# Optimization experiments

Hardware: AMD Instinct MI355X
Metric: run time of the kernel (lower is better)

The kernel has to match this reference:

```python
import jax, jax.numpy as jnp
import numpy as np

B, K, D = 512, 36, 1024
N_KERNELS = 4
OUT_DIM = 1024
OUT_PER_KERNEL = OUT_DIM // N_KERNELS  # 256


def setup_inputs() -> dict:
    key = jax.random.key(0)
    k1, k2, k3, k4, k5 = jax.random.split(key, 5)
    neighbourhood_features = jax.random.normal(k1, (B, K, D), dtype=jnp.float32)
    region_relation_weights = jax.random.uniform(k2, (B, K, K), dtype=jnp.float32)
    # Gaussian mixture params: init uniform(0, 1) as in init_parameters()
    mean_relation = jax.random.uniform(k3, (N_KERNELS,), dtype=jnp.float32)
    precision_relation = jax.random.uniform(k4, (N_KERNELS,), dtype=jnp.float32)
    # Per-kernel Linear weights (bias=False), torch default init U(-1/sqrt(D), 1/sqrt(D))
    bound = 1.0 / np.sqrt(D)
    W = jax.random.uniform(k5, (N_KERNELS, OUT_PER_KERNEL, D), dtype=jnp.float32,
                           minval=-bound, maxval=bound)
    return {
        "neighbourhood_features": neighbourhood_features,
        "region_relation_weights": region_relation_weights,
        "mean_relation": mean_relation,
        "precision_relation": precision_relation,
        "W": W,
    }


def reference(neighbourhood_features, region_relation_weights, mean_relation,
              precision_relation, W):
    b, k, d = neighbourhood_features.shape
    # Gaussian mixture edge weights, normalized over kernels: [B,K,K,n_kernels]
    diff = (region_relation_weights[..., None] - mean_relation) ** 2
    w = jnp.exp(-0.5 * diff / (1e-14 + precision_relation ** 2))
    w = w / jnp.sum(w, axis=-1, keepdims=True)
    # Original repeats feat[b,i] over the neighbour axis j, so
    # bmm(w^T, repeated_feat)[b,i,k,:] == (sum_j w[b,i,j,k]) * feat[b,i,:].
    # Exploit that linearity instead of materializing the [B,K,K,D] repeat.
    ws = jnp.sum(w, axis=2)  # [B,K,n_kernels]
    weighted = ws[..., None] * neighbourhood_features[:, :, None, :]  # [B,K,n,D]
    # Per-kernel linear (stacked): [B,K,n_kernels,out_per_kernel]
    out = jnp.einsum('bknd,nod->bkno', weighted, W)
    # Concatenate kernel outputs -> [B,K,out_feat_dim]
    return out.reshape(b, k, -1)
```

## Files before the change

kernel.cpp:

```cpp
#include <hip/hip_runtime.h>
#include <stdint.h>

#define BB   512
#define KNB  36
#define DD   1024
#define MM   (BB*KNB)
#define NN   1024

typedef float  f32x4  __attribute__((ext_vector_type(4)));
typedef __bf16 bf16x8 __attribute__((ext_vector_type(8)));
typedef unsigned short u16;
typedef unsigned int   u32;

__device__ __forceinline__ u16 f2bf(float f) {
    u32 u = __float_as_uint(f);
    u32 r = (u + 0x7fffu + ((u >> 16) & 1u)) >> 16;
    return (u16)r;
}

__device__ __forceinline__ void gld16(const void* g, void* l) {
    __builtin_amdgcn_global_load_lds(
        (const __attribute__((address_space(1))) u32*)g,
        (__attribute__((address_space(3))) u32*)l,
        16, 0, 0);
}

__device__ __forceinline__ void cast_chunk_swz(const float* __restrict__ in,
                                               u16* __restrict__ out,
                                               long long c, int r) {
    long long src = (c & ~7LL) | ((c & 7) ^ (r & 7));
    const f32x4* p = (const f32x4*)(in + src * 8);
    f32x4 v0 = p[0], v1 = p[1];
    union { u16 us[8]; uint4 u4; } pk;
    pk.us[0] = f2bf(v0.x); pk.us[1] = f2bf(v0.y);
    pk.us[2] = f2bf(v0.z); pk.us[3] = f2bf(v0.w);
    pk.us[4] = f2bf(v1.x); pk.us[5] = f2bf(v1.y);
    pk.us[6] = f2bf(v1.z); pk.us[7] = f2bf(v1.w);
    *((uint4*)(out + c * 8)) = pk.u4;
}

#define WS_BLOCKS   72
#define CW_BLOCKS   512
#define CA_BLOCKS   1152
#define CA_THREADS  (CA_BLOCKS * 256)
__global__ void prep_kernel(const float* __restrict__ rrw,
                            const float* __restrict__ mean,
                            const float* __restrict__ prec,
                            float* __restrict__ wsT,
                            const float* __restrict__ W,
                            u16* __restrict__ Wbf,
                            const float* __restrict__ A,
                            u16* __restrict__ Abf) {
    const int blk = blockIdx.x;
    if (blk < WS_BLOCKS) {
        int id = blk * 256 + threadIdx.x;
        float m0 = mean[0], m1 = mean[1], m2 = mean[2], m3 = mean[3];
        float i0 = 1.0f / (1e-14f + prec[0] * prec[0]);
        float i1 = 1.0f / (1e-14f + prec[1] * prec[1]);
        float i2 = 1.0f / (1e-14f + prec[2] * prec[2]);
        float i3 = 1.0f / (1e-14f + prec[3] * prec[3]);
        const float* p = rrw + (size_t)id * KNB;
        float a0 = 0.f, a1 = 0.f, a2 = 0.f, a3 = 0.f;
        for (int j = 0; j < KNB; ++j) {
            float x = p[j];
            float d0 = x - m0, d1 = x - m1, d2 = x - m2, d3 = x - m3;
            float e0 = expf(-0.5f * d0 * d0 * i0);
            float e1 = expf(-0.5f * d1 * d1 * i1);
            float e2 = expf(-0.5f * d2 * d2 * i2);
            float e3 = expf(-0.5f * d3 * d3 * i3);
            float inv = 1.0f / (e0 + e1 + e2 + e3);
            a0 += e0 * inv; a1 += e1 * inv; a2 += e2 * inv; a3 += e3 * inv;
        }
        wsT[0 * MM + id] = a0;
        wsT[1 * MM + id] = a1;
        wsT[2 * MM + id] = a2;
        wsT[3 * MM + id] = a3;
    } else if (blk < WS_BLOCKS + CW_BLOCKS) {
        long long c = (long long)(blk - WS_BLOCKS) * 256 + threadIdx.x;
        int r = (int)(c >> 7);
        cast_chunk_swz(W, Wbf, c, r);
    } else {
        long long t = (long long)(blk - WS_BLOCKS - CW_BLOCKS) * 256 + threadIdx.x;
#pragma unroll
        for (int k = 0; k < 8; ++k) {
            long long c = t + (long long)k * CA_THREADS;
            int r = (int)(c >> 7);
            cast_chunk_swz(A, Abf, c, r);
        }
    }
}

#define BM 128
#define BN 128
#define BK 64
#define KTILES (DD / BK)

#define VMCNT8()  asm volatile("s_waitcnt vmcnt(8)" ::: "memory")
#define VMCNT0()  asm volatile("s_waitcnt vmcnt(0)" ::: "memory")
#define BAR()     __builtin_amdgcn_s_barrier()

__global__ __launch_bounds__(256, 4) void gemm_kernel(
        const u16* __restrict__ A,
        const u16* __restrict__ Bm,
        const float* __restrict__ wsT,
        float* __restrict__ out) {
    __shared__ __align__(16) u16 As0[BM * BK];
    __shared__ __align__(16) u16 As1[BM * BK];
    __shared__ __align__(16) u16 Bs0[BN * BK];
    __shared__ __align__(16) u16 Bs1[BN * BK];

    const int tid = threadIdx.x;
    const int bid   = blockIdx.x;
    const int xcd   = bid & 7;
    const int local = bid >> 3;
    const int by    = xcd * 18 + (local >> 3);
    const int bx    = local & 7;
    const int rowBase = by * BM;
    const int colBase = bx * BN;
    const int lane = tid & 63;
    const int w    = tid >> 6;
    const int wr   = w >> 1;
    const int wc   = w & 1;
    const int fr   = lane & 15;
    const int fq   = lane >> 4;

    f32x4 acc[4][4];
#pragma unroll
    for (int m = 0; m < 4; ++m)
#pragma unroll
        for (int n = 0; n < 4; ++n)
            acc[m][n] = (f32x4)0.0f;

    const u16* aptr = A  + (size_t)(rowBase + (tid >> 3)) * DD + (tid & 7) * 8;
    const u16* bptr = Bm + (size_t)(colBase + (tid >> 3)) * DD + (tid & 7) * 8;

    auto STAGE = [&](u16* as, u16* bs, int kt) {
#pragma unroll
        for (int i = 0; i < 4; ++i) {
            gld16(aptr + (size_t)i * 32 * DD + kt * BK, &as[(i * 256 + tid) * 8]);
            gld16(bptr + (size_t)i * 32 * DD + kt * BK, &bs[(i * 256 + tid) * 8]);
        }
    };

    auto COMPUTE = [&](const u16* as, const u16* bs) {
#pragma unroll
        for (int kk = 0; kk < 2; ++kk) {
            bf16x8 af[4], bfv[4];
#pragma unroll
            for (int m = 0; m < 4; ++m) {
                int r = wr * 64 + m * 16 + fr;
                int g = kk * 4 + fq;
                af[m] = ((const bf16x8*)&as[r * BK])[g ^ (r & 7)];
            }
#pragma unroll
            for (int n = 0; n < 4; ++n) {
                int r = wc * 64 + n * 16 + fr;
                int g = kk * 4 + fq;
                bfv[n] = ((const bf16x8*)&bs[r * BK])[g ^ (r & 7)];
            }
#pragma unroll
            for (int m = 0; m < 4; ++m)
#pragma unroll
                for (int n = 0; n < 4; ++n)
                    acc[m][n] = __builtin_amdgcn_mfma_f32_16x16x32_bf16(
                        af[m], bfv[n], acc[m][n], 0, 0, 0);
        }
    };

    STAGE(As0, Bs0, 0);

    for (int k2 = 0; k2 < (KTILES - 2) / 2; ++k2) {
        STAGE(As1, Bs1, 2 * k2 + 1);
        VMCNT8();
        BAR();
        COMPUTE(As0, Bs0);
        BAR();
        STAGE(As0, Bs0, 2 * k2 + 2);
        VMCNT8();
        BAR();
        COMPUTE(As1, Bs1);
        BAR();
    }
    STAGE(As1, Bs1, KTILES - 1);
    VMCNT8();
    BAR();
    COMPUTE(As0, Bs0);
    VMCNT0();
    BAR();
    COMPUTE(As1, Bs1);

    const int kn = bx >> 1;
#pragma unroll
    for (int m = 0; m < 4; ++m) {
        int r0 = rowBase + wr * 64 + m * 16 + fq * 4;
        f32x4 s = *(const f32x4*)&wsT[(size_t)kn * MM + r0];
#pragma unroll
        for (int n = 0; n < 4; ++n) {
            int c = colBase + wc * 64 + n * 16 + fr;
            float* o = out + (size_t)r0 * NN + c;
            o[0 * NN] = acc[m][n][0] * s[0];
            o[1 * NN] = acc[m][n][1] * s[1];
            o[2 * NN] = acc[m][n][2] * s[2];
            o[3 * NN] = acc[m][n][3] * s[3];
        }
    }
}

extern "C" void kernel_launch(void* const* d_in, const int* in_sizes, int n_in,
                              void* d_out, int out_size, void* d_ws, size_t ws_size,
                              hipStream_t stream) {
    const float* feat = (const float*)d_in[0];
    const float* rrw  = (const float*)d_in[1];
    const float* mean = (const float*)d_in[2];
    const float* prec = (const float*)d_in[3];
    const float* W    = (const float*)d_in[4];
    float* out = (float*)d_out;

    char* ws = (char*)d_ws;
    float* wsT = (float*)ws;
    u16*   Wbf = (u16*)(ws + 294912);
    u16*   Abf = (u16*)(ws + 294912 + 2097152);

    prep_kernel<<<dim3(WS_BLOCKS + CW_BLOCKS + CA_BLOCKS), dim3(256), 0, stream>>>(
        rrw, mean, prec, wsT, W, Wbf, feat, Abf);
    gemm_kernel<<<dim3((MM / BM) * (NN / BN)), dim3(256), 0, stream>>>(Abf, Wbf, wsT, out);
}
```

Baseline: 72.80 us.

## Fuse fp32-to-bf16 activation cast into GEMM A-tile loads

Removes the separate prep pass that cast the 512x36x1024 fp32 features to bf16 in workspace. The GEMM now loads fp32 A rows into registers, converts them to bf16 and writes them into swizzled LDS after each compute step, while B still streams through global_load_lds. This drops a full write plus re-read of the bf16 activation copy. In exchange, A staging goes through registers, adding VGPR pressure (launch bounds lowered to 2 waves per SIMD) and extra waitcnt and barrier ordering in the pipeline.

```diff
diff --git a/kernel.cpp b/kernel.cpp
--- a/kernel.cpp
+++ b/kernel.cpp
@@ -23,6 +23,13 @@
         (const __attribute__((address_space(1))) u32*)g,
         (__attribute__((address_space(3))) u32*)l,
         16, 0, 0);
+}
+
+__device__ __forceinline__ bf16x8 cvt8(f32x4 lo, f32x4 hi) {
+    bf16x8 r;
+    r[0] = (__bf16)lo.x; r[1] = (__bf16)lo.y; r[2] = (__bf16)lo.z; r[3] = (__bf16)lo.w;
+    r[4] = (__bf16)hi.x; r[5] = (__bf16)hi.y; r[6] = (__bf16)hi.z; r[7] = (__bf16)hi.w;
+    return r;
 }
 
 __device__ __forceinline__ void cast_chunk_swz(const float* __restrict__ in,
@@ -41,16 +48,12 @@
 
 #define WS_BLOCKS   72
 #define CW_BLOCKS   512
-#define CA_BLOCKS   1152
-#define CA_THREADS  (CA_BLOCKS * 256)
 __global__ void prep_kernel(const float* __restrict__ rrw,
                             const float* __restrict__ mean,
                             const float* __restrict__ prec,
                             float* __restrict__ wsT,
                             const float* __restrict__ W,
-                            u16* __restrict__ Wbf,
-                            const float* __restrict__ A,
-                            u16* __restrict__ Abf) {
+                            u16* __restrict__ Wbf) {
     const int blk = blockIdx.x;
     if (blk < WS_BLOCKS) {
         int id = blk * 256 + threadIdx.x;
@@ -75,18 +78,10 @@
         wsT[1 * MM + id] = a1;
         wsT[2 * MM + id] = a2;
         wsT[3 * MM + id] = a3;
-    } else if (blk < WS_BLOCKS + CW_BLOCKS) {
+    } else {
         long long c = (long long)(blk - WS_BLOCKS) * 256 + threadIdx.x;
         int r = (int)(c >> 7);
         cast_chunk_swz(W, Wbf, c, r);
-    } else {
-        long long t = (long long)(blk - WS_BLOCKS - CW_BLOCKS) * 256 + threadIdx.x;
-#pragma unroll
-        for (int k = 0; k < 8; ++k) {
-            long long c = t + (long long)k * CA_THREADS;
-            int r = (int)(c >> 7);
-            cast_chunk_swz(A, Abf, c, r);
-        }
     }
 }
 
@@ -95,12 +90,13 @@
 #define BK 64
 #define KTILES (DD / BK)
 
-#define VMCNT8()  asm volatile("s_waitcnt vmcnt(8)" ::: "memory")
+#define VMCNT12() asm volatile("s_waitcnt vmcnt(12)" ::: "memory")
 #define VMCNT0()  asm volatile("s_waitcnt vmcnt(0)" ::: "memory")
+#define LGKM0()   asm volatile("s_waitcnt lgkmcnt(0)" ::: "memory")
 #define BAR()     __builtin_amdgcn_s_barrier()
 
-__global__ __launch_bounds__(256, 4) void gemm_kernel(
-        const u16* __restrict__ A,
+__global__ __launch_bounds__(256, 2) void gemm_kernel(
+        const float* __restrict__ A,
         const u16* __restrict__ Bm,
         const float* __restrict__ wsT,
         float* __restrict__ out) {
@@ -131,14 +127,31 @@
         for (int n = 0; n < 4; ++n)
             acc[m][n] = (f32x4)0.0f;
 
-    const u16* aptr = A  + (size_t)(rowBase + (tid >> 3)) * DD + (tid & 7) * 8;
-    const u16* bptr = Bm + (size_t)(colBase + (tid >> 3)) * DD + (tid & 7) * 8;
-
-    auto STAGE = [&](u16* as, u16* bs, int kt) {
+    const int ar0 = tid >> 3;
+    const int aj  = tid & 7;
+    const float* abase = A + (size_t)(rowBase + ar0) * DD + aj * 8;
+    const u16*   bptr  = Bm + (size_t)(colBase + ar0) * DD + aj * 8;
+
+    f32x4 ra[4][2];
+
+    auto ISSUE_B = [&](u16* bs, int kt) {
+#pragma unroll
+        for (int i = 0; i < 4; ++i)
+            gld16(bptr + (size_t)i * 32 * DD + kt * BK, &bs[(i * 256 + tid) * 8]);
+    };
+    auto ISSUE_A = [&](int kt) {
 #pragma unroll
         for (int i = 0; i < 4; ++i) {
-            gld16(aptr + (size_t)i * 32 * DD + kt * BK, &as[(i * 256 + tid) * 8]);
-            gld16(bptr + (size_t)i * 32 * DD + kt * BK, &bs[(i * 256 + tid) * 8]);
+            const float* src = abase + (size_t)i * 32 * DD + kt * BK;
+            ra[i][0] = *(const f32x4*)src;
+            ra[i][1] = *(const f32x4*)(src + 4);
+        }
+    };
+    auto WRITE_A = [&](u16* as) {
+#pragma unroll
+        for (int i = 0; i < 4; ++i) {
+            int r = i * 32 + ar0;
+            *(bf16x8*)&as[r * BK + (aj ^ (r & 7)) * 8] = cvt8(ra[i][0], ra[i][1]);
         }
     };
 
@@ -167,24 +180,37 @@
         }
     };
 
-    STAGE(As0, Bs0, 0);
+    ISSUE_B(Bs0, 0);
+    ISSUE_A(0);
+    WRITE_A(As0);
+    VMCNT0(); LGKM0();
+    BAR();
 
     for (int k2 = 0; k2 < (KTILES - 2) / 2; ++k2) {
-        STAGE(As1, Bs1, 2 * k2 + 1);
-        VMCNT8();
+        ISSUE_B(Bs1, 2 * k2 + 1);
+        ISSUE_A(2 * k2 + 1);
+        VMCNT12();
         BAR();
         COMPUTE(As0, Bs0);
-        BAR();
-        STAGE(As0, Bs0, 2 * k2 + 2);
-        VMCNT8();
+        WRITE_A(As1);
+        LGKM0();
+        BAR();
+        ISSUE_B(Bs0, 2 * k2 + 2);
+        ISSUE_A(2 * k2 + 2);
+        VMCNT12();
         BAR();
         COMPUTE(As1, Bs1);
+        WRITE_A(As0);
+        LGKM0();
         BAR();
     }
-    STAGE(As1, Bs1, KTILES - 1);
-    VMCNT8();
+    ISSUE_B(Bs1, KTILES - 1);
+    ISSUE_A(KTILES - 1);
+    VMCNT12();
     BAR();
     COMPUTE(As0, Bs0);
+    WRITE_A(As1);
+    LGKM0();
     VMCNT0();
     BAR();
     COMPUTE(As1, Bs1);
@@ -219,9 +245,8 @@
     char* ws = (char*)d_ws;
     float* wsT = (float*)ws;
     u16*   Wbf = (u16*)(ws + 294912);
-    u16*   Abf = (u16*)(ws + 294912 + 2097152);
-
-    prep_kernel<<<dim3(WS_BLOCKS + CW_BLOCKS + CA_BLOCKS), dim3(256), 0, stream>>>(
-        rrw, mean, prec, wsT, W, Wbf, feat, Abf);
-    gemm_kernel<<<dim3((MM / BM) * (NN / BN)), dim3(256), 0, stream>>>(Abf, Wbf, wsT, out);
-}
+
+    prep_kernel<<<dim3(WS_BLOCKS + CW_BLOCKS), dim3(256), 0, stream>>>(
+        rrw, mean, prec, wsT, W, Wbf);
+    gemm_kernel<<<dim3((MM / BM) * (NN / BN)), dim3(256), 0, stream>>>(feat, Wbf, wsT, out);
+}
```

Measured after the change: 79.80 us. +9.6%, slower.

## Single-buffer B tile in LDS, loading B just-in-time while double-buffering A

Applied to the files above, without the earlier changes.

Drops the second LDS buffer for the B (weight) tile. B for the current k-tile is now issued right before its compute and waited on fully, while A keeps double buffering with prefetch one tile ahead. This shrinks LDS per block and lowers the launch-bounds occupancy hint from 4 to 3. The catch is that B loads are no longer hidden behind the previous compute, so every iteration waits on global-to-LDS latency for B.

```diff
diff --git a/kernel.cpp b/kernel.cpp
--- a/kernel.cpp
+++ b/kernel.cpp
@@ -95,19 +95,18 @@
 #define BK 64
 #define KTILES (DD / BK)
 
-#define VMCNT8()  asm volatile("s_waitcnt vmcnt(8)" ::: "memory")
+#define VMCNT4()  asm volatile("s_waitcnt vmcnt(4)" ::: "memory")
 #define VMCNT0()  asm volatile("s_waitcnt vmcnt(0)" ::: "memory")
 #define BAR()     __builtin_amdgcn_s_barrier()
 
-__global__ __launch_bounds__(256, 4) void gemm_kernel(
+__global__ __launch_bounds__(256, 3) void gemm_kernel(
         const u16* __restrict__ A,
         const u16* __restrict__ Bm,
         const float* __restrict__ wsT,
         float* __restrict__ out) {
     __shared__ __align__(16) u16 As0[BM * BK];
     __shared__ __align__(16) u16 As1[BM * BK];
-    __shared__ __align__(16) u16 Bs0[BN * BK];
-    __shared__ __align__(16) u16 Bs1[BN * BK];
+    __shared__ __align__(16) u16 Bs [BN * BK];
 
     const int tid = threadIdx.x;
     const int bid   = blockIdx.x;
@@ -134,15 +133,18 @@
     const u16* aptr = A  + (size_t)(rowBase + (tid >> 3)) * DD + (tid & 7) * 8;
     const u16* bptr = Bm + (size_t)(colBase + (tid >> 3)) * DD + (tid & 7) * 8;
 
-    auto STAGE = [&](u16* as, u16* bs, int kt) {
-#pragma unroll
-        for (int i = 0; i < 4; ++i) {
+    auto STAGE_A = [&](u16* as, int kt) {
+#pragma unroll
+        for (int i = 0; i < 4; ++i)
             gld16(aptr + (size_t)i * 32 * DD + kt * BK, &as[(i * 256 + tid) * 8]);
-            gld16(bptr + (size_t)i * 32 * DD + kt * BK, &bs[(i * 256 + tid) * 8]);
-        }
     };
-
-    auto COMPUTE = [&](const u16* as, const u16* bs) {
+    auto STAGE_B = [&](int kt) {
+#pragma unroll
+        for (int i = 0; i < 4; ++i)
+            gld16(bptr + (size_t)i * 32 * DD + kt * BK, &Bs[(i * 256 + tid) * 8]);
+    };
+
+    auto COMPUTE = [&](const u16* as) {
 #pragma unroll
         for (int kk = 0; kk < 2; ++kk) {
             bf16x8 af[4], bfv[4];
@@ -156,7 +158,7 @@
             for (int n = 0; n < 4; ++n) {
                 int r = wc * 64 + n * 16 + fr;
                 int g = kk * 4 + fq;
-                bfv[n] = ((const bf16x8*)&bs[r * BK])[g ^ (r & 7)];
+                bfv[n] = ((const bf16x8*)&Bs[r * BK])[g ^ (r & 7)];
             }
 #pragma unroll
             for (int m = 0; m < 4; ++m)
@@ -167,27 +169,32 @@
         }
     };
 
-    STAGE(As0, Bs0, 0);
+    STAGE_A(As0, 0);
 
     for (int k2 = 0; k2 < (KTILES - 2) / 2; ++k2) {
-        STAGE(As1, Bs1, 2 * k2 + 1);
-        VMCNT8();
-        BAR();
-        COMPUTE(As0, Bs0);
-        BAR();
-        STAGE(As0, Bs0, 2 * k2 + 2);
-        VMCNT8();
-        BAR();
-        COMPUTE(As1, Bs1);
+        STAGE_B(2 * k2);
+        STAGE_A(As1, 2 * k2 + 1);
+        VMCNT4();
+        BAR();
+        COMPUTE(As0);
+        BAR();
+        STAGE_B(2 * k2 + 1);
+        STAGE_A(As0, 2 * k2 + 2);
+        VMCNT4();
+        BAR();
+        COMPUTE(As1);
         BAR();
     }
-    STAGE(As1, Bs1, KTILES - 1);
-    VMCNT8();
+    STAGE_B(KTILES - 2);
+    STAGE_A(As1, KTILES - 1);
+    VMCNT4();
     BAR();
-    COMPUTE(As0, Bs0);
+    COMPUTE(As0);
+    BAR();
+    STAGE_B(KTILES - 1);
     VMCNT0();
     BAR();
-    COMPUTE(As1, Bs1);
+    COMPUTE(As1);
 
     const int kn = bx >> 1;
 #pragma unroll
```

After: 67.57 us, median of 3. 1.08x faster.
